# Optimization experiments

Measured on AMD Instinct MI355X. Metric: run time of the kernel, lower is better.

Reference implementation:

```python
import jax, jax.numpy as jnp
import numpy as np

TAU = 0.1
EPS = 1e-20


def _gumbel_softmax_hard(logits, gumbels, tau):
    # logits: [4], gumbels: [B, S, 4]
    y_soft = jax.nn.softmax((logits + gumbels) / tau, axis=-1)
    y_hard = jax.nn.one_hot(jnp.argmax(y_soft, axis=-1), logits.shape[-1], dtype=y_soft.dtype)
    # straight-through estimator (matches F.gumbel_softmax(hard=True))
    return y_hard + y_soft - jax.lax.stop_gradient(y_soft)


def _forward(mean, outcomeA, outcomeB, BEVa, BEVb, kapa):
    B, _, S = outcomeA.shape
    g_key = jax.random.key(42)
    u = jax.random.uniform(g_key, (B, S, 4), dtype=mean.dtype)
    gumbels = -jnp.log(-jnp.log(u + EPS) + EPS)  # standard Gumbel(0,1) noise
    logits = jax.nn.log_softmax(mean)            # F.log_softmax(m)
    p = _gumbel_softmax_hard(logits, gumbels, TAU)          # [B, S, 4] one-hot (ST)
    mask = (jnp.arange(S)[None, :] < kapa[:, None]).astype(p.dtype)  # s < kapa[b]
    denom = kapa.astype(p.dtype)
    # STa[b] = (1/kapa[b]) * sum_{s<kapa[b]} outcomeA[b,:,s] @ p[b,s]
    sta = jnp.einsum('bks,bsk,bs->b', outcomeA, p, mask) / denom
    stb = jnp.einsum('bks,bsk,bs->b', outcomeB, p, mask) / denom
    return jax.nn.sigmoid(BEVb - BEVa + stb - sta)  # [B]


def setup_inputs() -> dict:
    key = jax.random.key(0)
    B, S = 16384, 256
    k = jax.random.split(key, 6)
    return {
        'outcomeA': jax.random.normal(k[0], (B, 4, S), dtype=jnp.float32),
        'outcomeB': jax.random.normal(k[1], (B, 4, S), dtype=jnp.float32),
        'BEVa': jax.random.normal(k[2], (B,), dtype=jnp.float32),
        'BEVb': jax.random.normal(k[3], (B,), dtype=jnp.float32),
        'kapa': jax.random.randint(k[4], (B,), 1, S + 1, dtype=jnp.int32),
        'batch_size': B,
        'features': jax.random.normal(k[5], (B, 35), dtype=jnp.float32),
        'mean': jnp.array([2.0, 1.0, 1.0, 1.0], dtype=jnp.float32),
    }


def reference(outcomeA, outcomeB, BEVa, BEVb, kapa, batch_size, features, mean):
    # features is dead code in the original forward (MLP commented out)
    del batch_size, features
    return _forward(mean, outcomeA, outcomeB, BEVa, BEVb, kapa)
```

## Files before the change

### kernel.cpp

```cpp
#include <hip/hip_runtime.h>
#include <stdint.h>
#include <math.h>


__device__ __forceinline__ uint32_t rotl32(uint32_t x, int r) {
    return (x << r) | (x >> (32 - r));
}

__device__ __forceinline__ uint32_t tf2x32_xor(uint32_t c0, uint32_t c1) {
    const uint32_t ks0 = 0u, ks1 = 42u, ks2 = 0x1BD11BF0u;
    uint32_t x0 = c0 + ks0, x1 = c1 + ks1;
#define TF_R(r) { x0 += x1; x1 = rotl32(x1, r); x1 ^= x0; }
    TF_R(13) TF_R(15) TF_R(26) TF_R(6)
    x0 += ks1; x1 += ks2 + 1u;
    TF_R(17) TF_R(29) TF_R(16) TF_R(24)
    x0 += ks2; x1 += ks0 + 2u;
    TF_R(13) TF_R(15) TF_R(26) TF_R(6)
    x0 += ks0; x1 += ks1 + 3u;
    TF_R(17) TF_R(29) TF_R(16) TF_R(24)
    x0 += ks1; x1 += ks2 + 4u;
    TF_R(13) TF_R(15) TF_R(26) TF_R(6)
    x0 += ks2; x1 += ks0 + 5u;
#undef TF_R
    return x0 ^ x1;
}

__device__ __forceinline__ float fast_w(uint32_t m ) {
    const float u  = (float)m * 0x1p-23f;
    const float wl = -__logf(u + 1e-20f);
    const float d  = (float)(0x800000u - m) * 0x1p-23f;
    const float d2 = d * d;
    const float ws = d + d2 * (0.5f + d * (0.333333333f + d * (0.25f + d * 0.2f)));
    return (u > 0.96875f) ? ws : wl;
}

__device__ __forceinline__ double exact_lw(uint32_t m) {
    const double u = (double)m * 0x1p-23;
    const double w = -log(u + 1e-20) + 1e-20;
    return log(w);
}

__global__ __launch_bounds__(256) void bayes_kernel(
    const float* __restrict__ A,
    const float* __restrict__ Bo,
    const float* __restrict__ BEVa,
    const float* __restrict__ BEVb,
    const int*   __restrict__ kapa,
    const float* __restrict__ mean,
    float*       __restrict__ out)
{
    const int wid  = threadIdx.x >> 6;
    const int lane = threadIdx.x & 63;
    const int b    = (blockIdx.x << 2) | wid;
    const int kp   = kapa[b];

    const float m0 = mean[0], m1 = mean[1], m2 = mean[2], m3 = mean[3];
    const float mx = fmaxf(fmaxf(m0, m1), fmaxf(m2, m3));
    const float c0 = m0 - mx, c1 = m1 - mx, c2 = m2 - mx, c3 = m3 - mx;
    const bool grouped = (c1 == c2) && (c2 == c3);

    const float* __restrict__ Arow = A  + (size_t)b * 1024;
    const float* __restrict__ Brow = Bo + (size_t)b * 1024;

    float av = 0.0f, bv = 0.0f;
#pragma unroll
    for (int j = 0; j < 4; ++j) {
        const int s = lane + (j << 6);
        if (s < kp) {
            const uint32_t i0 = ((uint32_t)(b * 256 + s)) << 2;
            uint32_t m[4];
#pragma unroll
            for (int k = 0; k < 4; ++k)
                m[k] = tf2x32_xor(0u, i0 + (uint32_t)k) >> 9;

            int ksel;
            if (grouped) {
                int jg = 1; uint32_t mm = m[1];
                if (m[2] > mm) { mm = m[2]; jg = 2; }
                if (m[3] > mm) { mm = m[3]; jg = 3; }
                const float s0f = c0 - __logf(fast_w(m[0]));
                const float sjf = c1 - __logf(fast_w(mm));
                ksel = (s0f >= sjf) ? 0 : jg;
                if (fabsf(s0f - sjf) < 5e-4f) {
                    const double S0 = (double)c0 - exact_lw(m[0]);
                    const double Sj = (double)c1 - exact_lw(mm);
                    ksel = (S0 >= Sj) ? 0 : jg;
                }
            } else {
                const float cc[4] = { c0, c1, c2, c3 };
                float sc[4];
#pragma unroll
                for (int k = 0; k < 4; ++k)
                    sc[k] = cc[k] - __logf(fast_w(m[k]));
                float b1 = sc[0], b2 = -3.4e38f; ksel = 0;
#pragma unroll
                for (int k = 1; k < 4; ++k) {
                    if (sc[k] > b1)      { b2 = b1; b1 = sc[k]; ksel = k; }
                    else if (sc[k] > b2) { b2 = sc[k]; }
                }
                if (b1 - b2 < 5e-4f) {
                    double best = -1.0e308; ksel = 0;
#pragma unroll
                    for (int k = 0; k < 4; ++k) {
                        const double sk = (double)cc[k] - exact_lw(m[k]);
                        if (sk > best) { best = sk; ksel = k; }
                    }
                }
            }
            const int off = (ksel << 8) + s;
            av += Arow[off];
            bv += Brow[off];
        }
    }

#pragma unroll
    for (int off = 32; off >= 1; off >>= 1) {
        av += __shfl_down(av, off);
        bv += __shfl_down(bv, off);
    }

    if (lane == 0) {
        const double d = (double)kp;
        const double x = (double)BEVb[b] - (double)BEVa[b]
                       + (double)bv / d - (double)av / d;
        out[b] = (float)(1.0 / (1.0 + exp(-x)));
    }
}

extern "C" void kernel_launch(void* const* d_in, const int* in_sizes, int n_in,
                              void* d_out, int out_size, void* d_ws, size_t ws_size,
                              hipStream_t stream) {
    (void)in_sizes; (void)n_in; (void)d_ws; (void)ws_size; (void)out_size;
    const float* A    = (const float*)d_in[0];
    const float* Bo   = (const float*)d_in[1];
    const float* BEVa = (const float*)d_in[2];
    const float* BEVb = (const float*)d_in[3];
    const int*   kapa = (const int*)d_in[4];
    const float* mean = (const float*)d_in[7];
    float* out = (float*)d_out;

    bayes_kernel<<<4096, 256, 0, stream>>>(A, Bo, BEVa, BEVb, kapa, mean, out);
}
```

Before: 158.7 us.

## Map one block per batch row and compare Gumbel scores in linear domain

Each batch row now gets its own 256-thread block, so each thread handles exactly one sequence position. Previously a single wavefront looped over four positions per row. Block results are combined through shared memory and a barrier. In the grouped-mean case, the two float log evaluations are replaced by a comparison of w values scaled by exp(c1-c0), with a relative tolerance that falls back to the exact double-precision path. This trades more blocks and a block-level sync for a shorter serial chain per thread and fewer transcendental calls.

```diff
diff --git a/kernel.cpp b/kernel.cpp
--- a/kernel.cpp
+++ b/kernel.cpp
@@ -49,68 +49,65 @@
     const float* __restrict__ mean,
     float*       __restrict__ out)
 {
-    const int wid  = threadIdx.x >> 6;
-    const int lane = threadIdx.x & 63;
-    const int b    = (blockIdx.x << 2) | wid;
-    const int kp   = kapa[b];
+    const int b  = blockIdx.x;
+    const int s  = threadIdx.x;
+    const int kp = kapa[b];
 
-    const float m0 = mean[0], m1 = mean[1], m2 = mean[2], m3 = mean[3];
-    const float mx = fmaxf(fmaxf(m0, m1), fmaxf(m2, m3));
-    const float c0 = m0 - mx, c1 = m1 - mx, c2 = m2 - mx, c3 = m3 - mx;
-    const bool grouped = (c1 == c2) && (c2 == c3);
+    int ksel = 0;
+    if (s < kp) {
+        const float m0f = mean[0], m1f = mean[1], m2f = mean[2], m3f = mean[3];
+        const float mx = fmaxf(fmaxf(m0f, m1f), fmaxf(m2f, m3f));
+        const float c0 = m0f - mx, c1 = m1f - mx, c2 = m2f - mx, c3 = m3f - mx;
+        const bool grouped = (c1 == c2) && (c2 == c3);
 
-    const float* __restrict__ Arow = A  + (size_t)b * 1024;
-    const float* __restrict__ Brow = Bo + (size_t)b * 1024;
+        const uint32_t i0 = ((uint32_t)(b * 256 + s)) << 2;
+        uint32_t m[4];
+#pragma unroll
+        for (int k = 0; k < 4; ++k)
+            m[k] = tf2x32_xor(0u, i0 + (uint32_t)k) >> 9;
+
+        if (grouped) {
+            int jg = 1; uint32_t mm = m[1];
+            if (m[2] > mm) { mm = m[2]; jg = 2; }
+            if (m[3] > mm) { mm = m[3]; jg = 3; }
+            const float K  = __expf(c1 - c0);
+            const float w0 = fast_w(m[0]);
+            const float wm = fast_w(mm);
+            const float t  = K * w0;
+            ksel = (wm >= t) ? 0 : jg;
+            if (fabsf(wm - t) < 4e-6f * (wm + t)) {
+                const double S0 = (double)c0 - exact_lw(m[0]);
+                const double Sj = (double)c1 - exact_lw(mm);
+                ksel = (S0 >= Sj) ? 0 : jg;
+            }
+        } else {
+            const float cc[4] = { c0, c1, c2, c3 };
+            float sc[4];
+#pragma unroll
+            for (int k = 0; k < 4; ++k)
+                sc[k] = cc[k] - __logf(fast_w(m[k]));
+            float b1 = sc[0], b2 = -3.4e38f; ksel = 0;
+#pragma unroll
+            for (int k = 1; k < 4; ++k) {
+                if (sc[k] > b1)      { b2 = b1; b1 = sc[k]; ksel = k; }
+                else if (sc[k] > b2) { b2 = sc[k]; }
+            }
+            if (b1 - b2 < 5e-4f) {
+                double best = -1.0e308; ksel = 0;
+#pragma unroll
+                for (int k = 0; k < 4; ++k) {
+                    const double sk = (double)cc[k] - exact_lw(m[k]);
+                    if (sk > best) { best = sk; ksel = k; }
+                }
+            }
+        }
+    }
 
     float av = 0.0f, bv = 0.0f;
-#pragma unroll
-    for (int j = 0; j < 4; ++j) {
-        const int s = lane + (j << 6);
-        if (s < kp) {
-            const uint32_t i0 = ((uint32_t)(b * 256 + s)) << 2;
-            uint32_t m[4];
-#pragma unroll
-            for (int k = 0; k < 4; ++k)
-                m[k] = tf2x32_xor(0u, i0 + (uint32_t)k) >> 9;
-
-            int ksel;
-            if (grouped) {
-                int jg = 1; uint32_t mm = m[1];
-                if (m[2] > mm) { mm = m[2]; jg = 2; }
-                if (m[3] > mm) { mm = m[3]; jg = 3; }
-                const float s0f = c0 - __logf(fast_w(m[0]));
-                const float sjf = c1 - __logf(fast_w(mm));
-                ksel = (s0f >= sjf) ? 0 : jg;
-                if (fabsf(s0f - sjf) < 5e-4f) {
-                    const double S0 = (double)c0 - exact_lw(m[0]);
-                    const double Sj = (double)c1 - exact_lw(mm);
-                    ksel = (S0 >= Sj) ? 0 : jg;
-                }
-            } else {
-                const float cc[4] = { c0, c1, c2, c3 };
-                float sc[4];
-#pragma unroll
-                for (int k = 0; k < 4; ++k)
-                    sc[k] = cc[k] - __logf(fast_w(m[k]));
-                float b1 = sc[0], b2 = -3.4e38f; ksel = 0;
-#pragma unroll
-                for (int k = 1; k < 4; ++k) {
-                    if (sc[k] > b1)      { b2 = b1; b1 = sc[k]; ksel = k; }
-                    else if (sc[k] > b2) { b2 = sc[k]; }
-                }
-                if (b1 - b2 < 5e-4f) {
-                    double best = -1.0e308; ksel = 0;
-#pragma unroll
-                    for (int k = 0; k < 4; ++k) {
-                        const double sk = (double)cc[k] - exact_lw(m[k]);
-                        if (sk > best) { best = sk; ksel = k; }
-                    }
-                }
-            }
-            const int off = (ksel << 8) + s;
-            av += Arow[off];
-            bv += Brow[off];
-        }
+    if (s < kp) {
+        const int off = (b * 4 + ksel) * 256 + s;
+        av = A[off];
+        bv = Bo[off];
     }
 
 #pragma unroll
@@ -119,10 +116,19 @@
         bv += __shfl_down(bv, off);
     }
 
-    if (lane == 0) {
+    __shared__ float red[4][2];
+    const int wid  = threadIdx.x >> 6;
+    const int lane = threadIdx.x & 63;
+    if (lane == 0) { red[wid][0] = av; red[wid][1] = bv; }
+    __syncthreads();
+
+    if (threadIdx.x == 0) {
+        float sA = 0.f, sB = 0.f;
+#pragma unroll
+        for (int w = 0; w < 4; ++w) { sA += red[w][0]; sB += red[w][1]; }
         const double d = (double)kp;
         const double x = (double)BEVb[b] - (double)BEVa[b]
-                       + (double)bv / d - (double)av / d;
+                       + (double)sB / d - (double)sA / d;
         out[b] = (float)(1.0 / (1.0 + exp(-x)));
     }
 }
@@ -139,5 +145,5 @@
     const float* mean = (const float*)d_in[7];
     float* out = (float*)d_out;
 
-    bayes_kernel<<<4096, 256, 0, stream>>>(A, Bo, BEVa, BEVb, kapa, mean, out);
+    bayes_kernel<<<16384, 256, 0, stream>>>(A, Bo, BEVa, BEVb, kapa, mean, out);
 }
```

Result: no change. 156.1 us (-1.6%).
